# Performance work log

Hardware: AMD Instinct MI355X
Metric: run time of the kernel (lower is better)

The kernel has to match this reference:

```python
import jax, jax.numpy as jnp
import numpy as np

B, N = 4, 256
EDGE_F = 256; NODE_F = 256; MSG = 128; LINK_H = 128
ROUNDS = 3; CLASSES = 600


def setup_inputs() -> dict:
    key = jax.random.key(0)
    ks = jax.random.split(key, 16)
    s = 0.05
    return {
        "edge_features": jax.random.normal(ks[0], (B, N, N, EDGE_F), jnp.float32),
        "node_features": jax.random.normal(ks[1], (B, N, NODE_F), jnp.float32),
        "adj_mat": jnp.zeros((B, N, N), jnp.float32),
        "node_labels": jnp.zeros((B, N, CLASSES), jnp.float32),
        "human_nums": jax.random.randint(ks[2], (B,), 0, 16),
        "obj_nums": jax.random.randint(ks[3], (B,), 0, 224),
        # feature-resize linears
        "W_er": jax.random.normal(ks[4], (EDGE_F, MSG), jnp.float32) * s,
        "b_er": jnp.zeros((MSG,), jnp.float32),
        "W_nr": jax.random.normal(ks[5], (NODE_F, MSG), jnp.float32) * s,
        "b_nr": jnp.zeros((MSG,), jnp.float32),
        # link function: 1x1 GraphConv stack MSG -> LINK_H -> 1
        "W_l1": jax.random.normal(ks[6], (MSG, LINK_H), jnp.float32) * s,
        "b_l1": jnp.zeros((LINK_H,), jnp.float32),
        "W_l2": jax.random.normal(ks[7], (LINK_H, 1), jnp.float32) * s,
        "b_l2": jnp.zeros((1,), jnp.float32),
        # message function: linear_concat_relu  (cat(h_w, e_vw) -> MSG)
        "W_msg": jax.random.normal(ks[8], (2 * MSG, MSG), jnp.float32) * s,
        "b_msg": jnp.zeros((MSG,), jnp.float32),
        # GRU update (torch gate order r,z,n)
        "W_ih": jax.random.normal(ks[9], (MSG, 3 * MSG), jnp.float32) * s,
        "b_ih": jnp.zeros((3 * MSG,), jnp.float32),
        "W_hh": jax.random.normal(ks[10], (MSG, 3 * MSG), jnp.float32) * s,
        "b_hh": jnp.zeros((3 * MSG,), jnp.float32),
        # readout fc
        "W_ro": jax.random.normal(ks[11], (MSG, CLASSES), jnp.float32) * s,
        "b_ro": jnp.zeros((CLASSES,), jnp.float32),
    }


def _gru_cell(x, h, W_ih, b_ih, W_hh, b_hh):
    gi = x @ W_ih + b_ih
    gh = h @ W_hh + b_hh
    ir, iz, i_n = jnp.split(gi, 3, axis=-1)
    hr, hz, h_n = jnp.split(gh, 3, axis=-1)
    r = jax.nn.sigmoid(ir + hr)
    z = jax.nn.sigmoid(iz + hz)
    n = jnp.tanh(i_n + r * h_n)
    return (1.0 - z) * n + z * h


def reference(edge_features, node_features, adj_mat, node_labels,
              human_nums, obj_nums,
              W_er, b_er, W_nr, b_nr, W_l1, b_l1, W_l2, b_l2,
              W_msg, b_msg, W_ih, b_ih, W_hh, b_hh, W_ro, b_ro):
    Bn, Nn = node_features.shape[0], node_features.shape[1]
    # resize_feature_to_message_size
    ef = edge_features @ W_er + b_er          # [B, N(i=receiver), N(w=sender), M]
    nf = node_features @ W_nr + b_nr          # [B, N, M]

    valid = (human_nums + obj_nums).astype(jnp.int32)
    node_mask = (jnp.arange(Nn)[None, :] < valid[:, None]).astype(ef.dtype)  # [B,N]
    pair_mask = node_mask[:, :, None] * node_mask[:, None, :]                # [B,N,N]

    # NOTE: the original forward never writes updated node states back into
    # hidden_node_states, so every round uses the ORIGINAL (resized) node and
    # edge features for the message function -> m_raw is round-invariant.
    cat = jnp.concatenate(
        [jnp.broadcast_to(nf[:, None, :, :], ef.shape), ef], axis=-1)  # [B,N,N,2M]
    m_raw = jax.nn.relu(cat @ W_msg + b_msg)                           # [B,N,N,M]

    e_state = ef                                    # hidden edge state, round 0
    pred_adj = jnp.zeros((Bn, Nn, Nn), ef.dtype)
    pred_labels = jnp.zeros((Bn, Nn, CLASSES), ef.dtype)
    for rnd in range(ROUNDS):
        # GraphConv link function (1x1 convs == per-edge MLP), valid block only
        hlink = jax.nn.relu(e_state @ W_l1 + b_l1)
        pred_adj = pair_mask * (hlink @ W_l2 + b_l2)[..., 0]     # [B,N,N]
        gate = jax.nn.sigmoid(pred_adj) * node_mask[:, None, :]  # zero invalid senders
        m = gate[..., None] * m_raw                              # [B,N,N,M]
        # next-round hidden edge state: column i holds gated messages to node i
        e_state = jnp.where(pair_mask[..., None] > 0, jnp.swapaxes(m, 1, 2), ef)
        if rnd == ROUNDS - 1:
            m_sum = m.sum(axis=2)                                # [B,N,M]
            h_new = _gru_cell(m_sum, nf, W_ih, b_ih, W_hh, b_hh)
            pred_labels = node_mask[..., None] * (h_new @ W_ro + b_ro)
    return pred_adj, pred_labels
```

## Files before the change

kernel.cpp:

```cpp
#include <hip/hip_runtime.h>
#include <hip/hip_bf16.h>


#define B_ 4
#define N_ 256
#define EF_ 256
#define M_ 128
#define CL_ 600
#define ADJ_SZ (B_*N_*N_)

typedef __hip_bfloat16 bf16;
typedef short short8 __attribute__((ext_vector_type(8)));
typedef float f32x4 __attribute__((ext_vector_type(4)));
typedef float fvec4 __attribute__((ext_vector_type(4)));

#define MFMA(a,b,c) __builtin_amdgcn_mfma_f32_16x16x32_bf16(a,b,c,0,0,0)

__device__ __forceinline__ float s2f(short s){
  union { unsigned int u; float f; } x; x.u = ((unsigned int)(unsigned short)s) << 16; return x.f;
}
__device__ __forceinline__ bf16 f2b(float f){ return __float2bfloat16(f); }
__device__ __forceinline__ float sigm(float x){ return 1.0f/(1.0f+expf(-x)); }

__device__ __forceinline__ float ldr(const void* p, size_t i, bool bf){
  return bf ? s2f(((const short*)p)[i]) : ((const float*)p)[i];
}
__device__ __forceinline__ void str(void* p, size_t i, float v, bool bf){
  if (bf) ((bf16*)p)[i] = f2b(v);
  else    ((float*)p)[i] = v;
}
__device__ __forceinline__ float dot8(short8 w, const float* x){
  float a = 0.f;
  #pragma unroll
  for (int j=0;j<8;j++) a += x[j]*s2f(w[j]);
  return a;
}

__global__ __launch_bounds__(64)
void k_detect(const unsigned short* ef, int* flag){
  int t = threadIdx.x;
  int cnt = 0;
  for (int j = 0; j < 64; j++){
    unsigned short u = ef[t*64 + j];
    int e = (u >> 7) & 0xFF;
    cnt += (e >= 96 && e <= 144) ? 1 : 0;
  }
  for (int o = 32; o > 0; o >>= 1) cnt += __shfl_down(cnt, o, 64);
  if (t == 0) *flag = (cnt > 3500) ? 1 : 0;
}

__global__ __launch_bounds__(256)
void k_prep(const void* W_er, const void* W_msg, const void* W_l1,
            const void* W_nr, const void* W_ih, const void* W_hh, const void* W_ro,
            bf16* pWer, bf16* pWmsgB, bf16* pWl1,
            bf16* tWnr, bf16* tWmsgT, bf16* tWih, bf16* tWhh, bf16* tWro,
            void* out, int out_size, const int* dflag)
{
  bool bf = (*dflag != 0);
  int nzb = (out_size + 255) >> 8;
  int blk = blockIdx.x;
  int t = threadIdx.x;
  if (blk < nzb){
    int i = blk*256 + t;
    if (i < out_size) str(out, i, 0.f, bf);
    return;
  }
  blk -= nzb;
  if (blk < 32){
    int unit = blk*4 + (t>>6);
    int lane = t & 63;
    const void* src; bf16* dst; int u2;
    if (unit < 64){ src = W_er; dst = pWer; u2 = unit; }
    else if (unit < 96){
      src = bf ? (const void*)((const short*)W_msg + 128*M_)
               : (const void*)((const float*)W_msg + 128*M_);
      dst = pWmsgB; u2 = unit - 64;
    } else { src = W_l1; dst = pWl1; u2 = unit - 96; }
    int kk = u2 >> 3, nt = u2 & 7;
    int k0 = kk*32 + (lane>>4)*8;
    int n  = nt*16 + (lane&15);
    size_t dbase = ((size_t)u2*64 + lane)*8;
    #pragma unroll
    for (int j=0;j<8;j++)
      dst[dbase+j] = f2b(ldr(src, (size_t)(k0+j)*128 + n, bf));
    return;
  }
  blk -= 32;
  int idx = blk*256 + t;
  const void* src; bf16* dst; int K, N;
  if (idx < 32768){ src = W_nr;  dst = tWnr;  K = 256; N = 128; }
  else if ((idx -= 32768) < 16384){ src = W_msg; dst = tWmsgT; K = 128; N = 128; }
  else if ((idx -= 16384) < 49152){ src = W_ih;  dst = tWih;  K = 128; N = 384; }
  else if ((idx -= 49152) < 49152){ src = W_hh;  dst = tWhh;  K = 128; N = 384; }
  else if ((idx -= 49152) < 76800){ src = W_ro;  dst = tWro;  K = 128; N = 600; }
  else return;
  int k = idx / N, n = idx % N;
  dst[(size_t)n*K + k] = f2b(ldr(src, idx, bf));
}

__global__ __launch_bounds__(128)
void k_nf_c(const void* nodef, const bf16* tWnr, const void* b_nr,
            const bf16* tWmsgT, const void* b_msg, float* nf, float* cb,
            const int* dflag)
{
  bool bf = (*dflag != 0);
  int blk = blockIdx.x; int b = blk >> 8; int v = blk & 255;
  int t = threadIdx.x;
  __shared__ float xs[EF_];
  __shared__ float nfs[M_];
  size_t xrow = ((size_t)(b*N_)+v)*EF_;
  xs[t]     = ldr(nodef, xrow + t, bf);
  xs[t+128] = ldr(nodef, xrow + t + 128, bf);
  __syncthreads();
  float acc = ldr(b_nr, t, bf);
  const short8* wp = (const short8*)(tWnr + (size_t)t*EF_);
  #pragma unroll 4
  for (int k8=0;k8<32;k8++) acc += dot8(wp[k8], &xs[k8*8]);
  nf[((size_t)(b*N_)+v)*M_+t] = acc;
  nfs[t] = acc;
  __syncthreads();
  float acc2 = ldr(b_msg, t, bf);
  const short8* wq = (const short8*)(tWmsgT + (size_t)t*M_);
  #pragma unroll 4
  for (int k8=0;k8<16;k8++) acc2 += dot8(wq[k8], &nfs[k8*8]);
  cb[((size_t)(b*N_)+v)*M_+t] = acc2;
}

__global__ __launch_bounds__(256)
void k_r0(const void* edgef, const bf16* pWer, const void* b_er,
          const bf16* pWmsgB, const float* cb, const bf16* pWl1,
          const void* b_l1, const void* W_l2, const void* b_l2,
          const int* hn, const int* on, bf16* mraw, float* u, float* s0,
          const int* dflag)
{
  bool bf = (*dflag != 0);
  int b = blockIdx.z, i = blockIdx.y, w0 = blockIdx.x*32;
  int valid = hn[b] + on[b];
  if (i >= valid || w0 >= valid) return;
  int t = threadIdx.x;
  __shared__ __attribute__((aligned(16))) bf16 EfsB[32][136];
  __shared__ __attribute__((aligned(16))) bf16 MrB[32][136];
  __shared__ __attribute__((aligned(16))) char uni[32*264*2];
  bf16  (*Xs)[264]  = (bf16(*)[264])uni;
  float (*hls)[132] = (float(*)[132])uni;

  {
    int j = t>>3, c = (t&7)*32;
    size_t g = (((size_t)(b*N_)+i)*N_ + (size_t)(w0+j))*EF_ + c;
    if (bf){
      const short8* src = (const short8*)((const short*)edgef + g);
      short8* dst = (short8*)&Xs[j][c];
      #pragma unroll
      for (int q=0;q<4;q++) dst[q] = src[q];
    } else {
      const fvec4* src = (const fvec4*)((const float*)edgef + g);
      #pragma unroll
      for (int q=0;q<8;q++){
        fvec4 v = src[q];
        #pragma unroll
        for (int e=0;e<4;e++) Xs[j][c+q*4+e] = f2b(v[e]);
      }
    }
  }
  __syncthreads();

  int lane = t & 63, wv = t >> 6;
  int r0 = (wv&1)*16;
  int c0h = wv >> 1;
  int mA = r0 + (lane&15);
  int kq = (lane>>4)*8;
  int qrow = r0 + (lane>>4)*4;

  f32x4 z4 = {0.f,0.f,0.f,0.f};
  f32x4 acc[4] = {z4,z4,z4,z4};
  for (int kk=0;kk<8;kk++){
    short8 a = *(const short8*)&Xs[mA][kk*32 + kq];
    #pragma unroll
    for (int nt=0;nt<4;nt++){
      int gnt = c0h*4 + nt;
      short8 bb = *(const short8*)(pWer + (((size_t)kk*8 + gnt)*64 + lane)*8);
      acc[nt] = MFMA(a, bb, acc[nt]);
    }
  }
  #pragma unroll
  for (int nt=0;nt<4;nt++){
    int col = c0h*64 + nt*16 + (lane&15);
    float be = ldr(b_er, col, bf);
    #pragma unroll
    for (int r=0;r<4;r++)
      EfsB[qrow+r][col] = f2b(acc[nt][r] + be);
  }
  __syncthreads();

  f32x4 am[4] = {z4,z4,z4,z4};
  f32x4 ah[4] = {z4,z4,z4,z4};
  for (int kk=0;kk<4;kk++){
    short8 a = *(const short8*)&EfsB[mA][kk*32 + kq];
    #pragma unroll
    for (int nt=0;nt<4;nt++){
      int gnt = c0h*4 + nt;
      size_t off = (((size_t)kk*8 + gnt)*64 + lane)*8;
      short8 b1 = *(const short8*)(pWmsgB + off);
      am[nt] = MFMA(a, b1, am[nt]);
      short8 b2 = *(const short8*)(pWl1 + off);
      ah[nt] = MFMA(a, b2, ah[nt]);
    }
  }
  #pragma unroll
  for (int nt=0;nt<4;nt++){
    int col = c0h*64 + nt*16 + (lane&15);
    float bl = ldr(b_l1, col, bf);
    #pragma unroll
    for (int r=0;r<4;r++){
      int row = qrow + r;
      int w = w0 + row;
      float v = am[nt][r] + cb[((size_t)(b*N_)+w)*M_ + col];
      bf16 mb = f2b(fmaxf(v, 0.f));
      mraw[(((size_t)(b*N_)+i)*N_ + w)*M_ + col] = mb;
      MrB[row][col] = mb;
      hls[row][col] = fmaxf(ah[nt][r] + bl, 0.f);
    }
  }
  __syncthreads();

  f32x4 au[4] = {z4,z4,z4,z4};
  for (int kk=0;kk<4;kk++){
    short8 a = *(const short8*)&MrB[mA][kk*32 + kq];
    #pragma unroll
    for (int nt=0;nt<4;nt++){
      short8 b2 = *(const short8*)(pWl1 + (((size_t)kk*8 + c0h*4 + nt)*64 + lane)*8);
      au[nt] = MFMA(a, b2, au[nt]);
    }
  }
  #pragma unroll
  for (int nt=0;nt<4;nt++){
    int col = c0h*64 + nt*16 + (lane&15);
    #pragma unroll
    for (int r=0;r<4;r++)
      u[(((size_t)(b*N_)+i)*N_ + (size_t)(w0+qrow+r))*M_ + col] = au[nt][r];
  }

  {
    int row = t>>3, seg = t&7;
    float p = 0.f;
    #pragma unroll
    for (int k=0;k<16;k++) p += hls[row][seg*16+k] * ldr(W_l2, seg*16+k, bf);
    p += __shfl_down(p, 4, 8);
    p += __shfl_down(p, 2, 8);
    p += __shfl_down(p, 1, 8);
    if (seg==0 && (w0+row) < valid)
      s0[((size_t)(b*N_)+i)*N_ + w0 + row] = p + ldr(b_l2, 0, bf);
  }
}

__global__ __launch_bounds__(256)
void k_linkE(const float* u, const float* s_prev, const void* b_l1,
             const void* W_l2, const void* b_l2,
             const int* hn, const int* on, float* s_next, const int* dflag)
{
  bool bf = (*dflag != 0);
  int i = blockIdx.x, b = blockIdx.y;
  int valid = hn[b] + on[b];
  if (i >= valid) return;
  int t = threadIdx.x;
  __shared__ float bl1s[M_], wl2s[M_];
  if (t < M_){ bl1s[t] = ldr(b_l1, t, bf); wl2s[t] = ldr(W_l2, t, bf); }
  __syncthreads();
  float bl2 = ldr(b_l2, 0, bf);
  int e = t>>3, seg = t&7;
  for (int w0 = 0; w0 < valid; w0 += 32){
    int w = w0 + e;
    if (w >= valid) break;
    float sg = sigm(s_prev[((size_t)(b*N_)+w)*N_ + i]);
    const fvec4* up = (const fvec4*)(u + (((size_t)(b*N_)+w)*N_ + i)*M_ + seg*16);
    float p = 0.f;
    #pragma unroll
    for (int q=0;q<4;q++){
      fvec4 v = up[q];
      #pragma unroll
      for (int e2=0;e2<4;e2++){
        int k = seg*16 + q*4 + e2;
        p += fmaxf(sg*v[e2] + bl1s[k], 0.f) * wl2s[k];
      }
    }
    p += __shfl_down(p, 4, 8);
    p += __shfl_down(p, 2, 8);
    p += __shfl_down(p, 1, 8);
    if (seg==0) s_next[((size_t)(b*N_)+i)*N_ + w] = p + bl2;
  }
}

__global__ __launch_bounds__(128)
void k_final(const bf16* mraw, const float* s2, const float* nf,
             const bf16* tWih, const void* b_ih,
             const bf16* tWhh, const void* b_hh,
             const bf16* tWro, const void* b_ro,
             const int* hn, const int* on, void* out, const int* dflag)
{
  bool bf = (*dflag != 0);
  int i = blockIdx.x, b = blockIdx.y;
  int valid = hn[b] + on[b];
  if (i >= valid) return;
  int t = threadIdx.x;
  __shared__ float sgs[N_];
  __shared__ float xsh[M_], hsh[M_], hns[M_];
  const float* srow = s2 + ((size_t)(b*N_)+i)*N_;
  size_t adj = ((size_t)(b*N_)+i)*N_;
  for (int w=t; w<N_; w+=128){
    if (w < valid){
      float v = srow[w];
      str(out, adj + w, v, bf);
      sgs[w] = sigm(v);
    } else sgs[w] = 0.f;
  }
  __syncthreads();
  const short* mrow = (const short*)mraw + (((size_t)(b*N_)+i)*N_)*M_;
  float acc = 0.f;
  for (int w=0; w<valid; w++) acc += sgs[w]*s2f(mrow[(size_t)w*M_ + t]);
  xsh[t] = acc;
  hsh[t] = nf[((size_t)(b*N_)+i)*M_ + t];
  __syncthreads();
  float gi[3], gh[3];
  #pragma unroll
  for (int g=0; g<3; g++){
    int o = g*M_ + t;
    float a = ldr(b_ih, o, bf), c = ldr(b_hh, o, bf);
    const short8* wi = (const short8*)(tWih + (size_t)o*M_);
    const short8* wh = (const short8*)(tWhh + (size_t)o*M_);
    #pragma unroll 4
    for (int k8=0;k8<16;k8++){
      a += dot8(wi[k8], &xsh[k8*8]);
      c += dot8(wh[k8], &hsh[k8*8]);
    }
    gi[g] = a; gh[g] = c;
  }
  float r  = sigm(gi[0] + gh[0]);
  float z  = sigm(gi[1] + gh[1]);
  float nn = tanhf(gi[2] + r*gh[2]);
  float hnew = (1.f - z)*nn + z*hsh[t];
  hns[t] = hnew;
  __syncthreads();
  size_t lab = (size_t)ADJ_SZ + ((size_t)(b*N_)+i)*CL_;
  for (int cls=t; cls<CL_; cls+=128){
    float a = ldr(b_ro, cls, bf);
    const short8* wr = (const short8*)(tWro + (size_t)cls*M_);
    #pragma unroll 4
    for (int k8=0;k8<16;k8++) a += dot8(wr[k8], &hns[k8*8]);
    str(out, lab + cls, a, bf);
  }
}

extern "C" void kernel_launch(void* const* d_in, const int* in_sizes, int n_in,
                              void* d_out, int out_size, void* d_ws, size_t ws_size,
                              hipStream_t stream)
{
  char* ws = (char*)d_ws;

  const void* edgef = d_in[0];
  const void* nodef = d_in[1];
  const int*  hn    = (const int*)d_in[4];
  const int*  on    = (const int*)d_in[5];
  const void* W_er  = d_in[6];  const void* b_er  = d_in[7];
  const void* W_nr  = d_in[8];  const void* b_nr  = d_in[9];
  const void* W_l1  = d_in[10]; const void* b_l1  = d_in[11];
  const void* W_l2  = d_in[12]; const void* b_l2  = d_in[13];
  const void* W_msg = d_in[14]; const void* b_msg = d_in[15];
  const void* W_ih  = d_in[16]; const void* b_ih  = d_in[17];
  const void* W_hh  = d_in[18]; const void* b_hh  = d_in[19];
  const void* W_ro  = d_in[20]; const void* b_ro  = d_in[21];

  bf16*  mraw   = (bf16*) (ws);
  float* uu     = (float*)(ws + 67108864);
  float* s_a    = (float*)(ws + 201326592);
  float* s_b    = (float*)(ws + 202375168);
  float* nf     = (float*)(ws + 203423744);
  float* cb     = (float*)(ws + 203948032);
  bf16*  pWer   = (bf16*) (ws + 204472320);
  bf16*  pWmsgB = (bf16*) (ws + 204537856);
  bf16*  pWl1   = (bf16*) (ws + 204570624);
  bf16*  tWnr   = (bf16*) (ws + 204603392);
  bf16*  tWmsgT = (bf16*) (ws + 204668928);
  bf16*  tWih   = (bf16*) (ws + 204701696);
  bf16*  tWhh   = (bf16*) (ws + 204800000);
  bf16*  tWro   = (bf16*) (ws + 204898304);
  int*   dflag  = (int*)  (ws + 205051904);

  k_detect<<<1, 64, 0, stream>>>((const unsigned short*)d_in[0], dflag);

  int nzb = (out_size + 255) / 256;
  k_prep<<<nzb + 32 + 876, 256, 0, stream>>>(
      W_er, W_msg, W_l1, W_nr, W_ih, W_hh, W_ro,
      pWer, pWmsgB, pWl1, tWnr, tWmsgT, tWih, tWhh, tWro,
      d_out, out_size, dflag);

  k_nf_c<<<B_*N_, 128, 0, stream>>>(nodef, tWnr, b_nr, tWmsgT, b_msg, nf, cb, dflag);

  dim3 g2(N_/32, N_, B_);
  k_r0<<<g2, 256, 0, stream>>>(edgef, pWer, b_er, pWmsgB, cb, pWl1,
                               b_l1, W_l2, b_l2, hn, on, mraw, uu, s_a, dflag);

  dim3 gl(N_, B_);
  k_linkE<<<gl, 256, 0, stream>>>(uu, s_a, b_l1, W_l2, b_l2, hn, on, s_b, dflag);
  k_linkE<<<gl, 256, 0, stream>>>(uu, s_b, b_l1, W_l2, b_l2, hn, on, s_a, dflag);

  k_final<<<gl, 128, 0, stream>>>(mraw, s_a, nf, tWih, b_ih, tWhh, b_hh,
                                  tWro, b_ro, hn, on, d_out, dflag);
}
```

Before: 512.7 us.

## Store link pre-activations in bf16, fuse last link round into final GRU/readout kernel

The per-edge link pre-activation buffer u is now stored in bf16 instead of fp32, halving its write and re-read traffic across rounds. The node-feature and concat-bias projections move into the prep kernel, reading the raw weights directly instead of pre-transposed bf16 copies. The last link round is fused with the gated message sum, GRU and readout into one kernel, removing a launch and an intermediate round trip. The trade-off is lower precision in u and uncached direct weight reads in the GEMV loops.

```diff
diff --git a/kernel.cpp b/kernel.cpp
--- a/kernel.cpp
+++ b/kernel.cpp
@@ -28,12 +28,6 @@
 __device__ __forceinline__ void str(void* p, size_t i, float v, bool bf){
   if (bf) ((bf16*)p)[i] = f2b(v);
   else    ((float*)p)[i] = v;
-}
-__device__ __forceinline__ float dot8(short8 w, const float* x){
-  float a = 0.f;
-  #pragma unroll
-  for (int j=0;j<8;j++) a += x[j]*s2f(w[j]);
-  return a;
 }
 
 __global__ __launch_bounds__(64)
@@ -51,11 +45,14 @@
 
 __global__ __launch_bounds__(256)
 void k_prep(const void* W_er, const void* W_msg, const void* W_l1,
-            const void* W_nr, const void* W_ih, const void* W_hh, const void* W_ro,
+            const void* nodef, const void* W_nr, const void* b_nr, const void* b_msg,
             bf16* pWer, bf16* pWmsgB, bf16* pWl1,
-            bf16* tWnr, bf16* tWmsgT, bf16* tWih, bf16* tWhh, bf16* tWro,
+            float* nf, float* cb,
             void* out, int out_size, const int* dflag)
 {
+  __shared__ float xs[EF_];
+  __shared__ float pp[2][M_];
+  __shared__ float nfs[M_];
   bool bf = (*dflag != 0);
   int nzb = (out_size + 255) >> 8;
   int blk = blockIdx.x;
@@ -86,51 +83,37 @@
     return;
   }
   blk -= 32;
-  int idx = blk*256 + t;
-  const void* src; bf16* dst; int K, N;
-  if (idx < 32768){ src = W_nr;  dst = tWnr;  K = 256; N = 128; }
-  else if ((idx -= 32768) < 16384){ src = W_msg; dst = tWmsgT; K = 128; N = 128; }
-  else if ((idx -= 16384) < 49152){ src = W_ih;  dst = tWih;  K = 128; N = 384; }
-  else if ((idx -= 49152) < 49152){ src = W_hh;  dst = tWhh;  K = 128; N = 384; }
-  else if ((idx -= 49152) < 76800){ src = W_ro;  dst = tWro;  K = 128; N = 600; }
-  else return;
-  int k = idx / N, n = idx % N;
-  dst[(size_t)n*K + k] = f2b(ldr(src, idx, bf));
-}
-
-__global__ __launch_bounds__(128)
-void k_nf_c(const void* nodef, const bf16* tWnr, const void* b_nr,
-            const bf16* tWmsgT, const void* b_msg, float* nf, float* cb,
-            const int* dflag)
-{
-  bool bf = (*dflag != 0);
-  int blk = blockIdx.x; int b = blk >> 8; int v = blk & 255;
-  int t = threadIdx.x;
-  __shared__ float xs[EF_];
-  __shared__ float nfs[M_];
+  if (blk >= 1024) return;
+  int b = blk >> 8, v = blk & 255;
+  int f = t & 127, h = t >> 7;
   size_t xrow = ((size_t)(b*N_)+v)*EF_;
-  xs[t]     = ldr(nodef, xrow + t, bf);
-  xs[t+128] = ldr(nodef, xrow + t + 128, bf);
-  __syncthreads();
-  float acc = ldr(b_nr, t, bf);
-  const short8* wp = (const short8*)(tWnr + (size_t)t*EF_);
-  #pragma unroll 4
-  for (int k8=0;k8<32;k8++) acc += dot8(wp[k8], &xs[k8*8]);
-  nf[((size_t)(b*N_)+v)*M_+t] = acc;
-  nfs[t] = acc;
-  __syncthreads();
-  float acc2 = ldr(b_msg, t, bf);
-  const short8* wq = (const short8*)(tWmsgT + (size_t)t*M_);
-  #pragma unroll 4
-  for (int k8=0;k8<16;k8++) acc2 += dot8(wq[k8], &nfs[k8*8]);
-  cb[((size_t)(b*N_)+v)*M_+t] = acc2;
+  xs[t] = ldr(nodef, xrow + t, bf);
+  __syncthreads();
+  float acc = 0.f;
+  for (int k = h*128; k < h*128+128; k++)
+    acc += xs[k]*ldr(W_nr, (size_t)k*M_ + f, bf);
+  pp[h][f] = acc;
+  __syncthreads();
+  if (h == 0){
+    float nv = pp[0][f] + pp[1][f] + ldr(b_nr, f, bf);
+    nf[((size_t)(b*N_)+v)*M_ + f] = nv;
+    nfs[f] = nv;
+  }
+  __syncthreads();
+  float acc2 = 0.f;
+  for (int k = h*64; k < h*64+64; k++)
+    acc2 += nfs[k]*ldr(W_msg, (size_t)k*M_ + f, bf);
+  pp[h][f] = acc2;
+  __syncthreads();
+  if (h == 0)
+    cb[((size_t)(b*N_)+v)*M_ + f] = pp[0][f] + pp[1][f] + ldr(b_msg, f, bf);
 }
 
 __global__ __launch_bounds__(256)
 void k_r0(const void* edgef, const bf16* pWer, const void* b_er,
           const bf16* pWmsgB, const float* cb, const bf16* pWl1,
           const void* b_l1, const void* W_l2, const void* b_l2,
-          const int* hn, const int* on, bf16* mraw, float* u, float* s0,
+          const int* hn, const int* on, bf16* mraw, bf16* ub, float* s0,
           const int* dflag)
 {
   bool bf = (*dflag != 0);
@@ -237,7 +220,7 @@
     int col = c0h*64 + nt*16 + (lane&15);
     #pragma unroll
     for (int r=0;r<4;r++)
-      u[(((size_t)(b*N_)+i)*N_ + (size_t)(w0+qrow+r))*M_ + col] = au[nt][r];
+      ub[(((size_t)(b*N_)+i)*N_ + (size_t)(w0+qrow+r))*M_ + col] = f2b(au[nt][r]);
   }
 
   {
@@ -254,7 +237,7 @@
 }
 
 __global__ __launch_bounds__(256)
-void k_linkE(const float* u, const float* s_prev, const void* b_l1,
+void k_linkE(const bf16* ub, const float* s_prev, const void* b_l1,
              const void* W_l2, const void* b_l2,
              const int* hn, const int* on, float* s_next, const int* dflag)
 {
@@ -272,16 +255,18 @@
     int w = w0 + e;
     if (w >= valid) break;
     float sg = sigm(s_prev[((size_t)(b*N_)+w)*N_ + i]);
-    const fvec4* up = (const fvec4*)(u + (((size_t)(b*N_)+w)*N_ + i)*M_ + seg*16);
+    const short8* up = (const short8*)(ub + (((size_t)(b*N_)+w)*N_ + i)*M_ + seg*16);
+    short8 v0 = up[0], v1 = up[1];
     float p = 0.f;
     #pragma unroll
-    for (int q=0;q<4;q++){
-      fvec4 v = up[q];
-      #pragma unroll
-      for (int e2=0;e2<4;e2++){
-        int k = seg*16 + q*4 + e2;
-        p += fmaxf(sg*v[e2] + bl1s[k], 0.f) * wl2s[k];
-      }
+    for (int q=0;q<8;q++){
+      int k = seg*16 + q;
+      p += fmaxf(sg*s2f(v0[q]) + bl1s[k], 0.f) * wl2s[k];
+    }
+    #pragma unroll
+    for (int q=0;q<8;q++){
+      int k = seg*16 + 8 + q;
+      p += fmaxf(sg*s2f(v1[q]) + bl1s[k], 0.f) * wl2s[k];
     }
     p += __shfl_down(p, 4, 8);
     p += __shfl_down(p, 2, 8);
@@ -290,11 +275,11 @@
   }
 }
 
-__global__ __launch_bounds__(128)
-void k_final(const bf16* mraw, const float* s2, const float* nf,
-             const bf16* tWih, const void* b_ih,
-             const bf16* tWhh, const void* b_hh,
-             const bf16* tWro, const void* b_ro,
+__global__ __launch_bounds__(256)
+void k_linkF(const bf16* ub, const float* s_prev, const bf16* mraw, const float* nf,
+             const void* b_l1, const void* W_l2, const void* b_l2,
+             const void* W_ih, const void* b_ih, const void* W_hh, const void* b_hh,
+             const void* W_ro, const void* b_ro,
              const int* hn, const int* on, void* out, const int* dflag)
 {
   bool bf = (*dflag != 0);
@@ -302,51 +287,82 @@
   int valid = hn[b] + on[b];
   if (i >= valid) return;
   int t = threadIdx.x;
+  __shared__ float bl1s[M_], wl2s[M_];
   __shared__ float sgs[N_];
+  __shared__ float pp[2][M_];
   __shared__ float xsh[M_], hsh[M_], hns[M_];
-  const float* srow = s2 + ((size_t)(b*N_)+i)*N_;
+  __shared__ float gout[768];
+  if (t < M_){ bl1s[t] = ldr(b_l1, t, bf); wl2s[t] = ldr(W_l2, t, bf); }
+  sgs[t] = 0.f;
+  __syncthreads();
+  float bl2 = ldr(b_l2, 0, bf);
   size_t adj = ((size_t)(b*N_)+i)*N_;
-  for (int w=t; w<N_; w+=128){
+  int e = t>>3, seg = t&7;
+  for (int w0 = 0; w0 < valid; w0 += 32){
+    int w = w0 + e;
     if (w < valid){
-      float v = srow[w];
-      str(out, adj + w, v, bf);
-      sgs[w] = sigm(v);
-    } else sgs[w] = 0.f;
-  }
-  __syncthreads();
-  const short* mrow = (const short*)mraw + (((size_t)(b*N_)+i)*N_)*M_;
+      float sg = sigm(s_prev[((size_t)(b*N_)+w)*N_ + i]);
+      const short8* up = (const short8*)(ub + (((size_t)(b*N_)+w)*N_ + i)*M_ + seg*16);
+      short8 v0 = up[0], v1 = up[1];
+      float p = 0.f;
+      #pragma unroll
+      for (int q=0;q<8;q++){
+        int k = seg*16 + q;
+        p += fmaxf(sg*s2f(v0[q]) + bl1s[k], 0.f) * wl2s[k];
+      }
+      #pragma unroll
+      for (int q=0;q<8;q++){
+        int k = seg*16 + 8 + q;
+        p += fmaxf(sg*s2f(v1[q]) + bl1s[k], 0.f) * wl2s[k];
+      }
+      p += __shfl_down(p, 4, 8);
+      p += __shfl_down(p, 2, 8);
+      p += __shfl_down(p, 1, 8);
+      if (seg == 0){
+        float s2v = p + bl2;
+        str(out, adj + w, s2v, bf);
+        sgs[w] = sigm(s2v);
+      }
+    }
+  }
+  __syncthreads();
+  int f = t & 127, h = t >> 7;
+  const short* mrow = (const short*)mraw + adj*M_;
   float acc = 0.f;
-  for (int w=0; w<valid; w++) acc += sgs[w]*s2f(mrow[(size_t)w*M_ + t]);
-  xsh[t] = acc;
-  hsh[t] = nf[((size_t)(b*N_)+i)*M_ + t];
-  __syncthreads();
-  float gi[3], gh[3];
+  for (int w = h; w < valid; w += 2)
+    acc += sgs[w]*s2f(mrow[(size_t)w*M_ + f]);
+  pp[h][f] = acc;
+  __syncthreads();
+  if (h == 0){
+    xsh[f] = pp[0][f] + pp[1][f];
+    hsh[f] = nf[((size_t)(b*N_)+i)*M_ + f];
+  }
+  __syncthreads();
   #pragma unroll
-  for (int g=0; g<3; g++){
-    int o = g*M_ + t;
-    float a = ldr(b_ih, o, bf), c = ldr(b_hh, o, bf);
-    const short8* wi = (const short8*)(tWih + (size_t)o*M_);
-    const short8* wh = (const short8*)(tWhh + (size_t)o*M_);
-    #pragma unroll 4
-    for (int k8=0;k8<16;k8++){
-      a += dot8(wi[k8], &xsh[k8*8]);
-      c += dot8(wh[k8], &hsh[k8*8]);
-    }
-    gi[g] = a; gh[g] = c;
-  }
-  float r  = sigm(gi[0] + gh[0]);
-  float z  = sigm(gi[1] + gh[1]);
-  float nn = tanhf(gi[2] + r*gh[2]);
-  float hnew = (1.f - z)*nn + z*hsh[t];
-  hns[t] = hnew;
+  for (int rep=0; rep<3; rep++){
+    int j = rep*256 + t;
+    int isH = (j >= 384);
+    int jj = isH ? (j-384) : j;
+    const void* W = isH ? W_hh : W_ih;
+    const void* bb = isH ? b_hh : b_ih;
+    const float* x = isH ? hsh : xsh;
+    float a = ldr(bb, jj, bf);
+    for (int k=0;k<128;k++) a += x[k]*ldr(W, (size_t)k*384 + jj, bf);
+    gout[j] = a;
+  }
+  __syncthreads();
+  if (t < 128){
+    float r  = sigm(gout[t]      + gout[384+t]);
+    float z  = sigm(gout[128+t]  + gout[512+t]);
+    float nn = tanhf(gout[256+t] + r*gout[640+t]);
+    hns[t] = (1.f - z)*nn + z*hsh[t];
+  }
   __syncthreads();
   size_t lab = (size_t)ADJ_SZ + ((size_t)(b*N_)+i)*CL_;
-  for (int cls=t; cls<CL_; cls+=128){
-    float a = ldr(b_ro, cls, bf);
-    const short8* wr = (const short8*)(tWro + (size_t)cls*M_);
-    #pragma unroll 4
-    for (int k8=0;k8<16;k8++) a += dot8(wr[k8], &hns[k8*8]);
-    str(out, lab + cls, a, bf);
+  for (int c=t; c<CL_; c+=256){
+    float a = ldr(b_ro, c, bf);
+    for (int k=0;k<128;k++) a += hns[k]*ldr(W_ro, (size_t)k*CL_ + c, bf);
+    str(out, lab + c, a, bf);
   }
 }
 
@@ -370,39 +386,30 @@
   const void* W_ro  = d_in[20]; const void* b_ro  = d_in[21];
 
   bf16*  mraw   = (bf16*) (ws);
-  float* uu     = (float*)(ws + 67108864);
-  float* s_a    = (float*)(ws + 201326592);
-  float* s_b    = (float*)(ws + 202375168);
-  float* nf     = (float*)(ws + 203423744);
-  float* cb     = (float*)(ws + 203948032);
-  bf16*  pWer   = (bf16*) (ws + 204472320);
-  bf16*  pWmsgB = (bf16*) (ws + 204537856);
-  bf16*  pWl1   = (bf16*) (ws + 204570624);
-  bf16*  tWnr   = (bf16*) (ws + 204603392);
-  bf16*  tWmsgT = (bf16*) (ws + 204668928);
-  bf16*  tWih   = (bf16*) (ws + 204701696);
-  bf16*  tWhh   = (bf16*) (ws + 204800000);
-  bf16*  tWro   = (bf16*) (ws + 204898304);
-  int*   dflag  = (int*)  (ws + 205051904);
+  bf16*  ub     = (bf16*) (ws + 67108864);
+  float* s_a    = (float*)(ws + 134217728);
+  float* s_b    = (float*)(ws + 135266304);
+  float* nf     = (float*)(ws + 136314880);
+  float* cb     = (float*)(ws + 136839168);
+  bf16*  pWer   = (bf16*) (ws + 137363456);
+  bf16*  pWmsgB = (bf16*) (ws + 137428992);
+  bf16*  pWl1   = (bf16*) (ws + 137461760);
+  int*   dflag  = (int*)  (ws + 137494528);
 
   k_detect<<<1, 64, 0, stream>>>((const unsigned short*)d_in[0], dflag);
 
   int nzb = (out_size + 255) / 256;
-  k_prep<<<nzb + 32 + 876, 256, 0, stream>>>(
-      W_er, W_msg, W_l1, W_nr, W_ih, W_hh, W_ro,
-      pWer, pWmsgB, pWl1, tWnr, tWmsgT, tWih, tWhh, tWro,
-      d_out, out_size, dflag);
-
-  k_nf_c<<<B_*N_, 128, 0, stream>>>(nodef, tWnr, b_nr, tWmsgT, b_msg, nf, cb, dflag);
+  k_prep<<<nzb + 32 + 1024, 256, 0, stream>>>(
+      W_er, W_msg, W_l1, nodef, W_nr, b_nr, b_msg,
+      pWer, pWmsgB, pWl1, nf, cb, d_out, out_size, dflag);
 
   dim3 g2(N_/32, N_, B_);
   k_r0<<<g2, 256, 0, stream>>>(edgef, pWer, b_er, pWmsgB, cb, pWl1,
-                               b_l1, W_l2, b_l2, hn, on, mraw, uu, s_a, dflag);
+                               b_l1, W_l2, b_l2, hn, on, mraw, ub, s_a, dflag);
 
   dim3 gl(N_, B_);
-  k_linkE<<<gl, 256, 0, stream>>>(uu, s_a, b_l1, W_l2, b_l2, hn, on, s_b, dflag);
-  k_linkE<<<gl, 256, 0, stream>>>(uu, s_b, b_l1, W_l2, b_l2, hn, on, s_a, dflag);
-
-  k_final<<<gl, 128, 0, stream>>>(mraw, s_a, nf, tWih, b_ih, tWhh, b_hh,
-                                  tWro, b_ro, hn, on, d_out, dflag);
-}
+  k_linkE<<<gl, 256, 0, stream>>>(ub, s_a, b_l1, W_l2, b_l2, hn, on, s_b, dflag);
+  k_linkF<<<gl, 256, 0, stream>>>(ub, s_b, mraw, nf, b_l1, W_l2, b_l2,
+                                  W_ih, b_ih, W_hh, b_hh, W_ro, b_ro,
+                                  hn, on, d_out, dflag);
+}
```

Result: slower. 619.8 us (+20.9%).

## Recompute link hidden layer from bf16 messages instead of storing fp32 u

Applied to the files above, without the earlier changes.

Rounds 1 and 2 previously precomputed u = m_raw @ W_l1 in fp32 (128 MB buffer) in k_r0 and read it back in k_linkE. The change drops that buffer and instead has a new tiled MFMA kernel k_linkM reload the bf16 m_raw tile (half the bytes), recompute the projection, and apply the sigmoid gate as a per-row scale. This trades extra matrix-core work for much less HBM write and read traffic, and shrinks the workspace.

```diff
diff --git a/kernel.cpp b/kernel.cpp
--- a/kernel.cpp
+++ b/kernel.cpp
@@ -130,7 +130,7 @@
 void k_r0(const void* edgef, const bf16* pWer, const void* b_er,
           const bf16* pWmsgB, const float* cb, const bf16* pWl1,
           const void* b_l1, const void* W_l2, const void* b_l2,
-          const int* hn, const int* on, bf16* mraw, float* u, float* s0,
+          const int* hn, const int* on, bf16* mraw, float* s0,
           const int* dflag)
 {
   bool bf = (*dflag != 0);
@@ -139,7 +139,6 @@
   if (i >= valid || w0 >= valid) return;
   int t = threadIdx.x;
   __shared__ __attribute__((aligned(16))) bf16 EfsB[32][136];
-  __shared__ __attribute__((aligned(16))) bf16 MrB[32][136];
   __shared__ __attribute__((aligned(16))) char uni[32*264*2];
   bf16  (*Xs)[264]  = (bf16(*)[264])uni;
   float (*hls)[132] = (float(*)[132])uni;
@@ -215,31 +214,11 @@
       int row = qrow + r;
       int w = w0 + row;
       float v = am[nt][r] + cb[((size_t)(b*N_)+w)*M_ + col];
-      bf16 mb = f2b(fmaxf(v, 0.f));
-      mraw[(((size_t)(b*N_)+i)*N_ + w)*M_ + col] = mb;
-      MrB[row][col] = mb;
+      mraw[(((size_t)(b*N_)+i)*N_ + w)*M_ + col] = f2b(fmaxf(v, 0.f));
       hls[row][col] = fmaxf(ah[nt][r] + bl, 0.f);
     }
   }
   __syncthreads();
-
-  f32x4 au[4] = {z4,z4,z4,z4};
-  for (int kk=0;kk<4;kk++){
-    short8 a = *(const short8*)&MrB[mA][kk*32 + kq];
-    #pragma unroll
-    for (int nt=0;nt<4;nt++){
-      short8 b2 = *(const short8*)(pWl1 + (((size_t)kk*8 + c0h*4 + nt)*64 + lane)*8);
-      au[nt] = MFMA(a, b2, au[nt]);
-    }
-  }
-  #pragma unroll
-  for (int nt=0;nt<4;nt++){
-    int col = c0h*64 + nt*16 + (lane&15);
-    #pragma unroll
-    for (int r=0;r<4;r++)
-      u[(((size_t)(b*N_)+i)*N_ + (size_t)(w0+qrow+r))*M_ + col] = au[nt][r];
-  }
-
   {
     int row = t>>3, seg = t&7;
     float p = 0.f;
@@ -254,39 +233,69 @@
 }
 
 __global__ __launch_bounds__(256)
-void k_linkE(const float* u, const float* s_prev, const void* b_l1,
-             const void* W_l2, const void* b_l2,
+void k_linkM(const bf16* mraw, const float* s_prev, const bf16* pWl1,
+             const void* b_l1, const void* W_l2, const void* b_l2,
              const int* hn, const int* on, float* s_next, const int* dflag)
 {
   bool bf = (*dflag != 0);
-  int i = blockIdx.x, b = blockIdx.y;
+  int b = blockIdx.z, i = blockIdx.y, w0 = blockIdx.x*32;
   int valid = hn[b] + on[b];
-  if (i >= valid) return;
-  int t = threadIdx.x;
-  __shared__ float bl1s[M_], wl2s[M_];
-  if (t < M_){ bl1s[t] = ldr(b_l1, t, bf); wl2s[t] = ldr(W_l2, t, bf); }
-  __syncthreads();
-  float bl2 = ldr(b_l2, 0, bf);
-  int e = t>>3, seg = t&7;
-  for (int w0 = 0; w0 < valid; w0 += 32){
-    int w = w0 + e;
-    if (w >= valid) break;
-    float sg = sigm(s_prev[((size_t)(b*N_)+w)*N_ + i]);
-    const fvec4* up = (const fvec4*)(u + (((size_t)(b*N_)+w)*N_ + i)*M_ + seg*16);
+  if (i >= valid || w0 >= valid) return;
+  int t = threadIdx.x;
+  __shared__ __attribute__((aligned(16))) bf16 Ms[32][136];
+  __shared__ __attribute__((aligned(16))) float hls[32][132];
+  __shared__ float sg[32];
+  if (t < 32){
+    int w = w0 + t;
+    sg[t] = (w < valid) ? sigm(s_prev[((size_t)(b*N_)+w)*N_ + i]) : 0.f;
+  }
+  {
+    int j = t>>3, c = (t&7)*16;
+    const short8* src = (const short8*)((const short*)mraw +
+        (((size_t)(b*N_)+(size_t)(w0+j))*N_ + i)*M_ + c);
+    short8* dst = (short8*)&Ms[j][c];
+    dst[0] = src[0]; dst[1] = src[1];
+  }
+  __syncthreads();
+
+  int lane = t & 63, wv = t >> 6;
+  int r0 = (wv&1)*16;
+  int c0h = wv >> 1;
+  int mA = r0 + (lane&15);
+  int kq = (lane>>4)*8;
+  int qrow = r0 + (lane>>4)*4;
+
+  f32x4 z4 = {0.f,0.f,0.f,0.f};
+  f32x4 ah[4] = {z4,z4,z4,z4};
+  for (int kk=0;kk<4;kk++){
+    short8 a = *(const short8*)&Ms[mA][kk*32 + kq];
+    #pragma unroll
+    for (int nt=0;nt<4;nt++){
+      short8 b2 = *(const short8*)(pWl1 + (((size_t)kk*8 + c0h*4 + nt)*64 + lane)*8);
+      ah[nt] = MFMA(a, b2, ah[nt]);
+    }
+  }
+  #pragma unroll
+  for (int nt=0;nt<4;nt++){
+    int col = c0h*64 + nt*16 + (lane&15);
+    float bl = ldr(b_l1, col, bf);
+    #pragma unroll
+    for (int r=0;r<4;r++){
+      int row = qrow + r;
+      hls[row][col] = fmaxf(sg[row]*ah[nt][r] + bl, 0.f);
+    }
+  }
+  __syncthreads();
+  {
+    int row = t>>3, seg = t&7;
     float p = 0.f;
     #pragma unroll
-    for (int q=0;q<4;q++){
-      fvec4 v = up[q];
-      #pragma unroll
-      for (int e2=0;e2<4;e2++){
-        int k = seg*16 + q*4 + e2;
-        p += fmaxf(sg*v[e2] + bl1s[k], 0.f) * wl2s[k];
-      }
-    }
+    for (int k=0;k<16;k++) p += hls[row][seg*16+k] * ldr(W_l2, seg*16+k, bf);
     p += __shfl_down(p, 4, 8);
     p += __shfl_down(p, 2, 8);
     p += __shfl_down(p, 1, 8);
-    if (seg==0) s_next[((size_t)(b*N_)+i)*N_ + w] = p + bl2;
+    if (seg==0 && (w0+row) < valid)
+      s_next[((size_t)(b*N_)+i)*N_ + w0 + row] = p + ldr(b_l2, 0, bf);
   }
 }
 
@@ -370,20 +379,19 @@
   const void* W_ro  = d_in[20]; const void* b_ro  = d_in[21];
 
   bf16*  mraw   = (bf16*) (ws);
-  float* uu     = (float*)(ws + 67108864);
-  float* s_a    = (float*)(ws + 201326592);
-  float* s_b    = (float*)(ws + 202375168);
-  float* nf     = (float*)(ws + 203423744);
-  float* cb     = (float*)(ws + 203948032);
-  bf16*  pWer   = (bf16*) (ws + 204472320);
-  bf16*  pWmsgB = (bf16*) (ws + 204537856);
-  bf16*  pWl1   = (bf16*) (ws + 204570624);
-  bf16*  tWnr   = (bf16*) (ws + 204603392);
-  bf16*  tWmsgT = (bf16*) (ws + 204668928);
-  bf16*  tWih   = (bf16*) (ws + 204701696);
-  bf16*  tWhh   = (bf16*) (ws + 204800000);
-  bf16*  tWro   = (bf16*) (ws + 204898304);
-  int*   dflag  = (int*)  (ws + 205051904);
+  float* s_a    = (float*)(ws + 67108864);
+  float* s_b    = (float*)(ws + 68157440);
+  float* nf     = (float*)(ws + 69206016);
+  float* cb     = (float*)(ws + 69730304);
+  bf16*  pWer   = (bf16*) (ws + 70254592);
+  bf16*  pWmsgB = (bf16*) (ws + 70320128);
+  bf16*  pWl1   = (bf16*) (ws + 70352896);
+  bf16*  tWnr   = (bf16*) (ws + 70385664);
+  bf16*  tWmsgT = (bf16*) (ws + 70451200);
+  bf16*  tWih   = (bf16*) (ws + 70483968);
+  bf16*  tWhh   = (bf16*) (ws + 70582272);
+  bf16*  tWro   = (bf16*) (ws + 70680576);
+  int*   dflag  = (int*)  (ws + 70834176);
 
   k_detect<<<1, 64, 0, stream>>>((const unsigned short*)d_in[0], dflag);
 
@@ -397,12 +405,12 @@
 
   dim3 g2(N_/32, N_, B_);
   k_r0<<<g2, 256, 0, stream>>>(edgef, pWer, b_er, pWmsgB, cb, pWl1,
-                               b_l1, W_l2, b_l2, hn, on, mraw, uu, s_a, dflag);
+                               b_l1, W_l2, b_l2, hn, on, mraw, s_a, dflag);
+
+  k_linkM<<<g2, 256, 0, stream>>>(mraw, s_a, pWl1, b_l1, W_l2, b_l2, hn, on, s_b, dflag);
+  k_linkM<<<g2, 256, 0, stream>>>(mraw, s_b, pWl1, b_l1, W_l2, b_l2, hn, on, s_a, dflag);
 
   dim3 gl(N_, B_);
-  k_linkE<<<gl, 256, 0, stream>>>(uu, s_a, b_l1, W_l2, b_l2, hn, on, s_b, dflag);
-  k_linkE<<<gl, 256, 0, stream>>>(uu, s_b, b_l1, W_l2, b_l2, hn, on, s_a, dflag);
-
   k_final<<<gl, 128, 0, stream>>>(mraw, s_a, nf, tWih, b_ih, tWhh, b_hh,
                                   tWro, b_ro, hn, on, d_out, dflag);
 }
```

New measurement: 539.3 us. +5.2%, slower.

## Store link intermediate u in bf16 and spread k_linkE over a 3D grid

Applied to the files above, without the earlier changes.

The per-edge link pre-activation u is now written in bf16 instead of fp32, which halves the traffic for writing it in k_r0 and reading it twice in k_linkE. k_linkE is also relaunched on the same (N/32, N, B) grid as k_r0, so each block handles 32 senders instead of looping over all of them. This gives many more blocks and more parallelism. The cost is bf16 rounding of u before the ReLU and W_l2 dot product, which adds error to the link logits.

```diff
diff --git a/kernel.cpp b/kernel.cpp
--- a/kernel.cpp
+++ b/kernel.cpp
@@ -130,7 +130,7 @@
 void k_r0(const void* edgef, const bf16* pWer, const void* b_er,
           const bf16* pWmsgB, const float* cb, const bf16* pWl1,
           const void* b_l1, const void* W_l2, const void* b_l2,
-          const int* hn, const int* on, bf16* mraw, float* u, float* s0,
+          const int* hn, const int* on, bf16* mraw, bf16* ub, float* s0,
           const int* dflag)
 {
   bool bf = (*dflag != 0);
@@ -237,7 +237,7 @@
     int col = c0h*64 + nt*16 + (lane&15);
     #pragma unroll
     for (int r=0;r<4;r++)
-      u[(((size_t)(b*N_)+i)*N_ + (size_t)(w0+qrow+r))*M_ + col] = au[nt][r];
+      ub[(((size_t)(b*N_)+i)*N_ + (size_t)(w0+qrow+r))*M_ + col] = f2b(au[nt][r]);
   }
 
   {
@@ -254,40 +254,39 @@
 }
 
 __global__ __launch_bounds__(256)
-void k_linkE(const float* u, const float* s_prev, const void* b_l1,
+void k_linkE(const bf16* ub, const float* s_prev, const void* b_l1,
              const void* W_l2, const void* b_l2,
              const int* hn, const int* on, float* s_next, const int* dflag)
 {
   bool bf = (*dflag != 0);
-  int i = blockIdx.x, b = blockIdx.y;
+  int b = blockIdx.z, i = blockIdx.y, w0 = blockIdx.x*32;
   int valid = hn[b] + on[b];
-  if (i >= valid) return;
+  if (i >= valid || w0 >= valid) return;
   int t = threadIdx.x;
   __shared__ float bl1s[M_], wl2s[M_];
   if (t < M_){ bl1s[t] = ldr(b_l1, t, bf); wl2s[t] = ldr(W_l2, t, bf); }
   __syncthreads();
-  float bl2 = ldr(b_l2, 0, bf);
   int e = t>>3, seg = t&7;
-  for (int w0 = 0; w0 < valid; w0 += 32){
-    int w = w0 + e;
-    if (w >= valid) break;
-    float sg = sigm(s_prev[((size_t)(b*N_)+w)*N_ + i]);
-    const fvec4* up = (const fvec4*)(u + (((size_t)(b*N_)+w)*N_ + i)*M_ + seg*16);
-    float p = 0.f;
-    #pragma unroll
-    for (int q=0;q<4;q++){
-      fvec4 v = up[q];
-      #pragma unroll
-      for (int e2=0;e2<4;e2++){
-        int k = seg*16 + q*4 + e2;
-        p += fmaxf(sg*v[e2] + bl1s[k], 0.f) * wl2s[k];
-      }
-    }
-    p += __shfl_down(p, 4, 8);
-    p += __shfl_down(p, 2, 8);
-    p += __shfl_down(p, 1, 8);
-    if (seg==0) s_next[((size_t)(b*N_)+i)*N_ + w] = p + bl2;
-  }
+  int w = w0 + e;
+  if (w >= valid) return;
+  float sg = sigm(s_prev[((size_t)(b*N_)+w)*N_ + i]);
+  const short8* up = (const short8*)(ub + (((size_t)(b*N_)+w)*N_ + i)*M_ + seg*16);
+  short8 v0 = up[0], v1 = up[1];
+  float p = 0.f;
+  #pragma unroll
+  for (int q=0;q<8;q++){
+    int k = seg*16 + q;
+    p += fmaxf(sg*s2f(v0[q]) + bl1s[k], 0.f) * wl2s[k];
+  }
+  #pragma unroll
+  for (int q=0;q<8;q++){
+    int k = seg*16 + 8 + q;
+    p += fmaxf(sg*s2f(v1[q]) + bl1s[k], 0.f) * wl2s[k];
+  }
+  p += __shfl_down(p, 4, 8);
+  p += __shfl_down(p, 2, 8);
+  p += __shfl_down(p, 1, 8);
+  if (seg==0) s_next[((size_t)(b*N_)+i)*N_ + w] = p + ldr(b_l2, 0, bf);
 }
 
 __global__ __launch_bounds__(128)
@@ -370,20 +369,20 @@
   const void* W_ro  = d_in[20]; const void* b_ro  = d_in[21];
 
   bf16*  mraw   = (bf16*) (ws);
-  float* uu     = (float*)(ws + 67108864);
-  float* s_a    = (float*)(ws + 201326592);
-  float* s_b    = (float*)(ws + 202375168);
-  float* nf     = (float*)(ws + 203423744);
-  float* cb     = (float*)(ws + 203948032);
-  bf16*  pWer   = (bf16*) (ws + 204472320);
-  bf16*  pWmsgB = (bf16*) (ws + 204537856);
-  bf16*  pWl1   = (bf16*) (ws + 204570624);
-  bf16*  tWnr   = (bf16*) (ws + 204603392);
-  bf16*  tWmsgT = (bf16*) (ws + 204668928);
-  bf16*  tWih   = (bf16*) (ws + 204701696);
-  bf16*  tWhh   = (bf16*) (ws + 204800000);
-  bf16*  tWro   = (bf16*) (ws + 204898304);
-  int*   dflag  = (int*)  (ws + 205051904);
+  bf16*  ub     = (bf16*) (ws + 67108864);
+  float* s_a    = (float*)(ws + 134217728);
+  float* s_b    = (float*)(ws + 135266304);
+  float* nf     = (float*)(ws + 136314880);
+  float* cb     = (float*)(ws + 136839168);
+  bf16*  pWer   = (bf16*) (ws + 137363456);
+  bf16*  pWmsgB = (bf16*) (ws + 137428992);
+  bf16*  pWl1   = (bf16*) (ws + 137461760);
+  bf16*  tWnr   = (bf16*) (ws + 137494528);
+  bf16*  tWmsgT = (bf16*) (ws + 137560064);
+  bf16*  tWih   = (bf16*) (ws + 137592832);
+  bf16*  tWhh   = (bf16*) (ws + 137691136);
+  bf16*  tWro   = (bf16*) (ws + 137789440);
+  int*   dflag  = (int*)  (ws + 137943040);
 
   k_detect<<<1, 64, 0, stream>>>((const unsigned short*)d_in[0], dflag);
 
@@ -397,12 +396,12 @@
 
   dim3 g2(N_/32, N_, B_);
   k_r0<<<g2, 256, 0, stream>>>(edgef, pWer, b_er, pWmsgB, cb, pWl1,
-                               b_l1, W_l2, b_l2, hn, on, mraw, uu, s_a, dflag);
+                               b_l1, W_l2, b_l2, hn, on, mraw, ub, s_a, dflag);
+
+  k_linkE<<<g2, 256, 0, stream>>>(ub, s_a, b_l1, W_l2, b_l2, hn, on, s_b, dflag);
+  k_linkE<<<g2, 256, 0, stream>>>(ub, s_b, b_l1, W_l2, b_l2, hn, on, s_a, dflag);
 
   dim3 gl(N_, B_);
-  k_linkE<<<gl, 256, 0, stream>>>(uu, s_a, b_l1, W_l2, b_l2, hn, on, s_b, dflag);
-  k_linkE<<<gl, 256, 0, stream>>>(uu, s_b, b_l1, W_l2, b_l2, hn, on, s_a, dflag);
-
   k_final<<<gl, 128, 0, stream>>>(mraw, s_a, nf, tWih, b_ih, tWhh, b_hh,
                                   tWro, b_ro, hn, on, d_out, dflag);
 }
```

Result: faster. 502.6 us (-2.0%).
